# Kernel tuning notes

Hardware: AMD Instinct MI355X
Metric: run time of the kernel (lower is better)

The kernel has to match this reference:

```python
import jax, jax.numpy as jnp
import numpy as np

N_NODES = 100000
N_EDGES = 1600000
D = 128
N_LAYERS = 4
N_GRAPHS = 512


def setup_inputs() -> dict:
    key = jax.random.key(0)
    ks = jax.random.split(key, 12)
    x = jax.random.normal(ks[0], (N_NODES, D), dtype=jnp.float32)
    edge_index = jax.random.randint(ks[1], (2, N_EDGES), 0, N_NODES, dtype=jnp.int64)
    batch = jnp.sort(jax.random.randint(ks[2], (N_NODES,), 0, N_GRAPHS, dtype=jnp.int64))
    scale = 1.0 / np.sqrt(D)
    Ws = jax.random.normal(ks[3], (N_LAYERS, D, D), dtype=jnp.float32) * scale
    bs = jnp.zeros((N_LAYERS, D), dtype=jnp.float32)
    mlp_w1 = jax.random.normal(ks[4], (D, 100), dtype=jnp.float32) * scale
    mlp_b1 = jnp.zeros((100,), dtype=jnp.float32)
    mlp_w2 = jax.random.normal(ks[5], (100, 4), dtype=jnp.float32) * (1.0 / np.sqrt(100.0))
    mlp_b2 = jnp.zeros((4,), dtype=jnp.float32)
    return {"x": x, "Ws": Ws, "bs": bs, "mlp_w1": mlp_w1, "mlp_b1": mlp_b1,
            "mlp_w2": mlp_w2, "mlp_b2": mlp_b2, "edge_index": edge_index, "batch": batch}


def _gcn_conv(x, W, b, row, col, norm):
    # x: [N, Din]; W: [Din, Dout]. PyG GCNConv: linear, then normalized scatter-add.
    xw = x @ W                                # [N, Dout]
    msg = xw[row] * norm[:, None]             # gather at source nodes [E', Dout]
    out = jax.ops.segment_sum(msg, col, num_segments=N_NODES)
    return out + b


def reference(x, Ws, bs, mlp_w1, mlp_b1, mlp_w2, mlp_b2, edge_index, batch):
    # Add self-loops and compute symmetric normalization (once; shared by all layers).
    loop = jnp.arange(N_NODES, dtype=edge_index.dtype)
    row = jnp.concatenate([edge_index[0], loop])  # source
    col = jnp.concatenate([edge_index[1], loop])  # target
    deg = jax.ops.segment_sum(jnp.ones_like(col, dtype=x.dtype), col, num_segments=N_NODES)
    dinv = jnp.where(deg > 0, jax.lax.rsqrt(deg), 0.0)
    norm = dinv[row] * dinv[col]              # [E']

    h = x
    for i in range(N_LAYERS - 1):
        # dropout is identity in eval mode
        h = _gcn_conv(h, Ws[i], bs[i], row, col, norm)
        h = jax.nn.relu(h)
    h = _gcn_conv(h, Ws[-1], bs[-1], row, col, norm)

    # global mean pool over graphs
    sums = jax.ops.segment_sum(h, batch, num_segments=N_GRAPHS)
    counts = jax.ops.segment_sum(jnp.ones((N_NODES,), dtype=h.dtype), batch, num_segments=N_GRAPHS)
    pooled = sums / jnp.maximum(counts, 1.0)[:, None]  # [G, D]

    # MLP head: D -> 100 -> 4 (relu between, dropout identity in eval)
    hid = jax.nn.relu(pooled @ mlp_w1 + mlp_b1)
    pred = hid @ mlp_w2 + mlp_b2
    return pred
```

## Files before the change

### kernel.cpp

```cpp
#include <hip/hip_runtime.h>

#define N_NODES  100000
#define N_EDGES  1600000
#define DIM      128
#define N_GRAPHS 512

#define BW       512
#define NBUCK    ((N_NODES + BW - 1) / BW)
#define CAP      12288
#define NB_CHUNK 4096

typedef short  bf16x8 __attribute__((ext_vector_type(8)));
typedef float  f32x4  __attribute__((ext_vector_type(4)));

__device__ inline ushort f2bf(float f) {
    union { float f; unsigned u; } v; v.f = f;
    unsigned r = v.u + 0x7FFFu + ((v.u >> 16) & 1u);
    return (ushort)(r >> 16);
}
__device__ inline float bf2f_lo(unsigned u) { union { unsigned u; float f; } v; v.u = u << 16; return v.f; }
__device__ inline float bf2f_hi(unsigned u) { union { unsigned u; float f; } v; v.u = u & 0xFFFF0000u; return v.f; }


__global__ __launch_bounds__(256) void setup_kernel(const float* __restrict__ Ws,
                                                    ushort* __restrict__ WT,
                                                    int* __restrict__ bfill,
                                                    int* __restrict__ csr) {
    int idx = blockIdx.x * 256 + threadIdx.x;
    int L = idx >> 14, n = (idx >> 7) & 127, k = idx & 127;
    WT[idx] = f2bf(Ws[(L << 14) + (k << 7) + n]);
    if (blockIdx.x == 0) {
        int t = threadIdx.x;
        if (t < NBUCK) bfill[t] = t * CAP;
        if (t == 255) csr[N_NODES] = N_EDGES;
    }
}


__global__ __launch_bounds__(1024) void bin_kernel(const int* __restrict__ row,
                                                   const int* __restrict__ col,
                                                   int* __restrict__ bfill,
                                                   unsigned* __restrict__ tmp) {
    __shared__ unsigned s_val[NB_CHUNK];
    __shared__ int s_dst[NB_CHUNK];
    __shared__ int s_hist[256], s_scan[256];
    __shared__ int s_excl[NBUCK], s_base[NBUCK], s_cur[NBUCK];
    int t = threadIdx.x;
    int e0 = blockIdx.x * NB_CHUNK;

    if (t < 256) s_hist[t] = 0;
    __syncthreads();
#pragma unroll
    for (int k = 0; k < 4; ++k) {
        int e = e0 + t + k * 1024;
        if (e < N_EDGES) atomicAdd(&s_hist[col[e] >> 9], 1);
    }
    __syncthreads();
    int h = 0;
    if (t < 256) { h = s_hist[t]; s_scan[t] = h; }
    __syncthreads();
    for (int o = 1; o < 256; o <<= 1) {
        int u = 0;
        if (t < 256 && t >= o) u = s_scan[t - o];
        __syncthreads();
        if (t < 256) s_scan[t] += u;
        __syncthreads();
    }
    if (t < NBUCK) {
        int ex = s_scan[t] - h;
        s_excl[t] = ex;
        s_cur[t]  = ex;
        s_base[t] = atomicAdd(&bfill[t], h);
    }
    __syncthreads();
#pragma unroll
    for (int k = 0; k < 4; ++k) {
        int e = e0 + t + k * 1024;
        if (e < N_EDGES) {
            int r = row[e], c = col[e];
            int b = c >> 9;
            int p = atomicAdd(&s_cur[b], 1);
            int dst = s_base[b] + (p - s_excl[b]);
            int lim = (b + 1) * CAP;
            if (dst >= lim) dst = lim - 1;
            s_val[p] = ((unsigned)(c & (BW - 1)) << 17) | (unsigned)r;
            s_dst[p] = dst;
        }
    }
    __syncthreads();
    int sc = N_EDGES - e0; if (sc > NB_CHUNK) sc = NB_CHUNK;
#pragma unroll
    for (int k = 0; k < 4; ++k) {
        int j = t + k * 1024;
        if (j < sc) tmp[s_dst[j]] = s_val[j];
    }
}

__global__ __launch_bounds__(1024) void sort_kernel(const unsigned* __restrict__ tmp,
                                                    const int* __restrict__ bfill,
                                                    int* __restrict__ csr,
                                                    float* __restrict__ dinv,
                                                    int* __restrict__ ssrc) {
    __shared__ int s_cnt[BW];
    __shared__ int s_pair[256];
    __shared__ int s_off[BW];
    __shared__ int s_cur[BW];
    __shared__ int s_bb[256];
    __shared__ int s_stage[CAP];
    int b = blockIdx.x, t = threadIdx.x;
    int wbeg = b * BW;
    int wn = N_NODES - wbeg; if (wn > BW) wn = BW;
    int nE = bfill[b] - b * CAP; if (nE > CAP) nE = CAP;
    const unsigned* T = tmp + (size_t)b * CAP;

    if (t < 256) {
        int c0 = 0;
        if (t < NBUCK) {
            c0 = bfill[t] - t * CAP;
            if (c0 > CAP) c0 = CAP;
        }
        s_bb[t] = c0;
    }
    __syncthreads();
    for (int o = 1; o < 256; o <<= 1) {
        int u = 0;
        if (t < 256 && t >= o) u = s_bb[t - o];
        __syncthreads();
        if (t < 256) s_bb[t] += u;
        __syncthreads();
    }
    int base = s_bb[b] - nE;

    for (int i = t; i < BW; i += 1024) s_cnt[i] = 0;
    __syncthreads();
    for (int i = t; i < nE; i += 1024) atomicAdd(&s_cnt[T[i] >> 17], 1);
    __syncthreads();
    int a0 = 0, a1 = 0;
    if (t < 256) { a0 = s_cnt[2 * t]; a1 = s_cnt[2 * t + 1]; s_pair[t] = a0 + a1; }
    __syncthreads();
    for (int o = 1; o < 256; o <<= 1) {
        int u = 0;
        if (t < 256 && t >= o) u = s_pair[t - o];
        __syncthreads();
        if (t < 256) s_pair[t] += u;
        __syncthreads();
    }
    if (t < 256) {
        int pre = s_pair[t] - (a0 + a1);
        s_off[2 * t] = pre;      s_off[2 * t + 1] = pre + a0;
        s_cur[2 * t] = pre;      s_cur[2 * t + 1] = pre + a0;
    }
    __syncthreads();
    for (int i = t; i < wn; i += 1024) {
        csr[wbeg + i]  = base + s_off[i];
        dinv[wbeg + i] = rsqrtf((float)(s_cnt[i] + 1));
    }
    for (int i = t; i < nE; i += 1024) {
        unsigned v = T[i];
        int p = atomicAdd(&s_cur[v >> 17], 1);
        s_stage[p] = (int)(v & 0x1FFFFu);
    }
    __syncthreads();
    for (int i = t; i < nE; i += 1024) ssrc[base + i] = s_stage[i];
}


__global__ __launch_bounds__(256) void cvt_x(const float* __restrict__ x,
                                             const float* __restrict__ dinv,
                                             ushort* __restrict__ xb,
                                             const int* __restrict__ batch,
                                             int* __restrict__ gstart) {
    int i = (blockIdx.x * 256 + threadIdx.x) * 4;
    float d = dinv[i >> 7];
    float4 v = *(const float4*)(x + i);
    ushort4 o;
    o.x = f2bf(v.x * d); o.y = f2bf(v.y * d); o.z = f2bf(v.z * d); o.w = f2bf(v.w * d);
    *(ushort4*)(xb + i) = o;

    int n = blockIdx.x * 256 + threadIdx.x;
    if (n < N_NODES) {
        int b  = batch[n];
        int bp = (n == 0) ? -1 : batch[n - 1];
        for (int g = bp + 1; g <= b; ++g) gstart[g] = n;
        if (n == N_NODES - 1) {
            for (int g = b + 1; g <= N_GRAPHS; ++g) gstart[g] = N_NODES;
        }
    }
}

#define ACC8(vv) do { \
    acc[0] += bf2f_lo((vv).x); acc[1] += bf2f_hi((vv).x); \
    acc[2] += bf2f_lo((vv).y); acc[3] += bf2f_hi((vv).y); \
    acc[4] += bf2f_lo((vv).z); acc[5] += bf2f_hi((vv).z); \
    acc[6] += bf2f_lo((vv).w); acc[7] += bf2f_hi((vv).w); } while (0)

__global__ __launch_bounds__(512) void layer_kernel(const ushort* __restrict__ g,
                                                    const ushort* __restrict__ WT,
                                                    const float* __restrict__ bias,
                                                    const float* __restrict__ dinv,
                                                    const int* __restrict__ csr,
                                                    const int* __restrict__ ssrc,
                                                    ushort* __restrict__ out,
                                                    int mode) {
    __shared__ ushort sW[128 * 128];
    __shared__ ushort sA[8][16 * 128];
    int t = threadIdx.x;
    int m0blk = blockIdx.x * 128;

    {
#pragma unroll
        for (int j = 0; j < 4; ++j) {
            int idx = t + j * 512;
            int r = idx >> 4, c = idx & 15;
            uint4 v = *(const uint4*)(WT + (size_t)r * 128 + c * 8);
            *(uint4*)(sW + r * 128 + ((c + r) & 15) * 8) = v;
        }
    }
    __syncthreads();

    int wv   = t >> 6;
    int lane = t & 63;
    int q    = lane >> 4;
    int l    = lane & 15;
    int mw   = m0blk + wv * 16;
    ushort* sAw = sA[wv];
    const uint4* hp = (const uint4*)g;

#pragma unroll 1
    for (int i = 0; i < 4; ++i) {
        int row  = q * 4 + i;
        int node = mw + row;
        float acc[8];
#pragma unroll
        for (int z = 0; z < 8; ++z) acc[z] = 0.f;
        if (node < N_NODES) {
            uint4 v = hp[(size_t)node * 16 + l];
            acc[0] = bf2f_lo(v.x); acc[1] = bf2f_hi(v.x);
            acc[2] = bf2f_lo(v.y); acc[3] = bf2f_hi(v.y);
            acc[4] = bf2f_lo(v.z); acc[5] = bf2f_hi(v.z);
            acc[6] = bf2f_lo(v.w); acc[7] = bf2f_hi(v.w);
            int e = csr[node], end = csr[node + 1];
            for (; e + 7 < end; e += 8) {
                int s0 = ssrc[e],     s1 = ssrc[e + 1], s2 = ssrc[e + 2], s3 = ssrc[e + 3];
                int s4 = ssrc[e + 4], s5 = ssrc[e + 5], s6 = ssrc[e + 6], s7 = ssrc[e + 7];
                uint4 v0 = hp[(size_t)s0 * 16 + l];
                uint4 v1 = hp[(size_t)s1 * 16 + l];
                uint4 v2 = hp[(size_t)s2 * 16 + l];
                uint4 v3 = hp[(size_t)s3 * 16 + l];
                uint4 v4 = hp[(size_t)s4 * 16 + l];
                uint4 v5 = hp[(size_t)s5 * 16 + l];
                uint4 v6 = hp[(size_t)s6 * 16 + l];
                uint4 v7 = hp[(size_t)s7 * 16 + l];
                ACC8(v0); ACC8(v1); ACC8(v2); ACC8(v3);
                ACC8(v4); ACC8(v5); ACC8(v6); ACC8(v7);
            }
            for (; e + 1 < end; e += 2) {
                int s0 = ssrc[e], s1 = ssrc[e + 1];
                uint4 v0 = hp[(size_t)s0 * 16 + l];
                uint4 v1 = hp[(size_t)s1 * 16 + l];
                ACC8(v0); ACC8(v1);
            }
            if (e < end) {
                int s = ssrc[e];
                uint4 v1 = hp[(size_t)s * 16 + l];
                ACC8(v1);
            }
            float d = dinv[node];
#pragma unroll
            for (int z = 0; z < 8; ++z) acc[z] *= d;
        }
        uint4 ov;
        ov.x = (uint)f2bf(acc[0]) | ((uint)f2bf(acc[1]) << 16);
        ov.y = (uint)f2bf(acc[2]) | ((uint)f2bf(acc[3]) << 16);
        ov.z = (uint)f2bf(acc[4]) | ((uint)f2bf(acc[5]) << 16);
        ov.w = (uint)f2bf(acc[6]) | ((uint)f2bf(acc[7]) << 16);
        *(uint4*)(sAw + row * 128 + ((l + row) & 15) * 8) = ov;
    }

    f32x4 facc[8];
#pragma unroll
    for (int n = 0; n < 8; ++n) facc[n] = (f32x4){0.f, 0.f, 0.f, 0.f};
#pragma unroll
    for (int ki = 0; ki < 4; ++ki) {
        int ca = ki * 4 + q;
        bf16x8 a = *(const bf16x8*)(sAw + l * 128 + ((ca + l) & 15) * 8);
#pragma unroll
        for (int n = 0; n < 8; ++n) {
            int rB = n * 16 + l;
            bf16x8 b = *(const bf16x8*)(sW + rB * 128 + ((ca + rB) & 15) * 8);
            facc[n] = __builtin_amdgcn_mfma_f32_16x16x32_bf16(a, b, facc[n], 0, 0, 0);
        }
    }

    {
        int lr0 = q * 4;
        float sc[4];
#pragma unroll
        for (int r = 0; r < 4; ++r) {
            int m = mw + lr0 + r;
            sc[r] = (mode && m < N_NODES) ? dinv[m] : 1.0f;
        }
#pragma unroll
        for (int n = 0; n < 8; ++n) {
            int col = n * 16 + l;
            float bv = bias[col];
            int c = col >> 3;
#pragma unroll
            for (int r = 0; r < 4; ++r) {
                int lr = lr0 + r;
                float v = facc[n][r] + bv;
                if (mode) v = fmaxf(v, 0.f) * sc[r];
                sAw[lr * 128 + ((c + lr) & 15) * 8 + (col & 7)] = f2bf(v);
            }
        }
    }
#pragma unroll
    for (int j = 0; j < 4; ++j) {
        int idx = lane + j * 64;
        int lr = idx >> 4, c = idx & 15;
        int m = mw + lr;
        if (m < N_NODES) {
            uint4 v = *(const uint4*)(sAw + lr * 128 + ((c + lr) & 15) * 8);
            *(uint4*)(out + (size_t)m * 128 + c * 8) = v;
        }
    }
}


__global__ __launch_bounds__(256) void pool_mlp(const ushort* __restrict__ h,
                                                const int* __restrict__ gstart,
                                                const float* __restrict__ w1,
                                                const float* __restrict__ b1,
                                                const float* __restrict__ w2,
                                                const float* __restrict__ b2,
                                                float* __restrict__ out) {
    __shared__ float part[4][128];
    __shared__ float mean[128];
    __shared__ float hid[100];
    int g = blockIdx.x;
    int s = gstart[g], e2 = gstart[g + 1];
    int p     = threadIdx.x & 63;
    int which = threadIdx.x >> 6;
    const uint* hu = (const uint*)h;

    float a0 = 0.f, a1 = 0.f;
    for (int n = s + which; n < e2; n += 4) {
        uint v = hu[(size_t)n * 64 + p];
        a0 += bf2f_lo(v);
        a1 += bf2f_hi(v);
    }
    part[which][2 * p]     = a0;
    part[which][2 * p + 1] = a1;
    __syncthreads();
    if (which == 0) {
        float c = fmaxf((float)(e2 - s), 1.0f);
        mean[2 * p]     = (part[0][2 * p] + part[1][2 * p] + part[2][2 * p] + part[3][2 * p]) / c;
        mean[2 * p + 1] = (part[0][2 * p + 1] + part[1][2 * p + 1] + part[2][2 * p + 1] + part[3][2 * p + 1]) / c;
    }
    __syncthreads();
    int t = threadIdx.x;
    if (t < 100) {
        float s1 = b1[t];
        for (int k = 0; k < 128; ++k) s1 = fmaf(mean[k], w1[k * 100 + t], s1);
        hid[t] = fmaxf(s1, 0.f);
    }
    __syncthreads();
    if (t < 4) {
        float s2 = b2[t];
        for (int j = 0; j < 100; ++j) s2 = fmaf(hid[j], w2[j * 4 + t], s2);
        out[(size_t)g * 4 + t] = s2;
    }
}


extern "C" void kernel_launch(void* const* d_in, const int* in_sizes, int n_in,
                              void* d_out, int out_size, void* d_ws, size_t ws_size,
                              hipStream_t stream) {
    const float* x   = (const float*)d_in[0];
    const float* Ws  = (const float*)d_in[1];
    const float* bs  = (const float*)d_in[2];
    const float* w1  = (const float*)d_in[3];
    const float* b1  = (const float*)d_in[4];
    const float* w2  = (const float*)d_in[5];
    const float* b2  = (const float*)d_in[6];
    const int*   ei  = (const int*)d_in[7];
    const int*   bat = (const int*)d_in[8];
    float* outp = (float*)d_out;

    char* p = (char*)d_ws;
    auto take = [&](size_t bytes) -> void* {
        void* r = (void*)p;
        p += (bytes + 255) & ~(size_t)255;
        return r;
    };
    int*      csr    = (int*)take((size_t)(N_NODES + 1) * 4);
    float*    dinv   = (float*)take((size_t)N_NODES * 4);
    int*      bfill  = (int*)take((size_t)NBUCK * 4);
    unsigned* tmp    = (unsigned*)take((size_t)NBUCK * CAP * 4);
    int*      ssrc   = (int*)take((size_t)N_EDGES * 4);
    ushort*   xb     = (ushort*)take((size_t)N_NODES * 128 * 2);
    ushort*   hbA    = (ushort*)take((size_t)N_NODES * 128 * 2);
    ushort*   hbB    = (ushort*)take((size_t)N_NODES * 128 * 2);
    ushort*   WT     = (ushort*)take((size_t)4 * 128 * 128 * 2);
    int*      gstart = (int*)take((size_t)(N_GRAPHS + 1) * 4);

    const int* row = ei;
    const int* col = ei + N_EDGES;

    setup_kernel<<<256, 256, 0, stream>>>(Ws, WT, bfill, csr);
    bin_kernel<<<(N_EDGES + NB_CHUNK - 1) / NB_CHUNK, 1024, 0, stream>>>(row, col, bfill, tmp);
    sort_kernel<<<NBUCK, 1024, 0, stream>>>(tmp, bfill, csr, dinv, ssrc);
    cvt_x<<<12500, 256, 0, stream>>>(x, dinv, xb, bat, gstart);

    const ushort* hin = xb;
    ushort* hout = hbA;
    for (int L = 0; L < 4; ++L) {
        layer_kernel<<<(N_NODES + 127) / 128, 512, 0, stream>>>(
            hin, WT + (size_t)L * 128 * 128, bs + (size_t)L * 128, dinv,
            csr, ssrc, hout, (L < 3) ? 1 : 0);
        hin = hout;
        hout = (hout == hbA) ? hbB : hbA;
    }
    pool_mlp<<<N_GRAPHS, 256, 0, stream>>>(hin, gstart, w1, b1, w2, b2, outp);
}
```

Baseline: 450.7 us.

## Merge front-end kernels, fuse mean pooling into last layer, scale by dinv in gather

Binning, x conversion to bf16 and weight transposition now run as one front kernel with block-range dispatch, so the cvt_x launch no longer waits on the sort. Because x is now converted before dinv exists, layer 0 applies the source dinv per edge inside the gather. The last layer no longer writes its output; it segment-sums rows per graph into a float accumulator with atomics, and a small MLP head kernel reads those sums. This trades the final activation write and the pool kernel's re-read for global atomics and an extra dinv load per edge in layer 0.

```diff
diff --git a/kernel.cpp b/kernel.cpp
--- a/kernel.cpp
+++ b/kernel.cpp
@@ -10,6 +10,10 @@
 #define CAP      12288
 #define NB_CHUNK 4096
 
+#define FB_BIN   ((N_EDGES + NB_CHUNK - 1) / NB_CHUNK)
+#define FB_CVT   3125
+#define FB_WT    64
+
 typedef short  bf16x8 __attribute__((ext_vector_type(8)));
 typedef float  f32x4  __attribute__((ext_vector_type(4)));
 
@@ -20,79 +24,93 @@
 }
 __device__ inline float bf2f_lo(unsigned u) { union { unsigned u; float f; } v; v.u = u << 16; return v.f; }
 __device__ inline float bf2f_hi(unsigned u) { union { unsigned u; float f; } v; v.u = u & 0xFFFF0000u; return v.f; }
-
-
-__global__ __launch_bounds__(256) void setup_kernel(const float* __restrict__ Ws,
-                                                    ushort* __restrict__ WT,
-                                                    int* __restrict__ bfill,
-                                                    int* __restrict__ csr) {
-    int idx = blockIdx.x * 256 + threadIdx.x;
-    int L = idx >> 14, n = (idx >> 7) & 127, k = idx & 127;
-    WT[idx] = f2bf(Ws[(L << 14) + (k << 7) + n]);
-    if (blockIdx.x == 0) {
-        int t = threadIdx.x;
-        if (t < NBUCK) bfill[t] = t * CAP;
-        if (t == 255) csr[N_NODES] = N_EDGES;
-    }
-}
-
-
-__global__ __launch_bounds__(1024) void bin_kernel(const int* __restrict__ row,
-                                                   const int* __restrict__ col,
-                                                   int* __restrict__ bfill,
-                                                   unsigned* __restrict__ tmp) {
+__device__ inline float bf2f_s(ushort u)    { union { unsigned u; float f; } v; v.u = (unsigned)u << 16; return v.f; }
+
+__global__ __launch_bounds__(1024) void front_kernel(const int* __restrict__ row,
+                                                     const int* __restrict__ col,
+                                                     int* __restrict__ bfill,
+                                                     unsigned* __restrict__ tmp,
+                                                     const float* __restrict__ x,
+                                                     ushort* __restrict__ xb,
+                                                     const int* __restrict__ batch,
+                                                     int* __restrict__ gstart,
+                                                     const float* __restrict__ Ws,
+                                                     ushort* __restrict__ WT) {
     __shared__ unsigned s_val[NB_CHUNK];
     __shared__ int s_dst[NB_CHUNK];
     __shared__ int s_hist[256], s_scan[256];
     __shared__ int s_excl[NBUCK], s_base[NBUCK], s_cur[NBUCK];
     int t = threadIdx.x;
-    int e0 = blockIdx.x * NB_CHUNK;
-
-    if (t < 256) s_hist[t] = 0;
-    __syncthreads();
-#pragma unroll
-    for (int k = 0; k < 4; ++k) {
-        int e = e0 + t + k * 1024;
-        if (e < N_EDGES) atomicAdd(&s_hist[col[e] >> 9], 1);
-    }
-    __syncthreads();
-    int h = 0;
-    if (t < 256) { h = s_hist[t]; s_scan[t] = h; }
-    __syncthreads();
-    for (int o = 1; o < 256; o <<= 1) {
-        int u = 0;
-        if (t < 256 && t >= o) u = s_scan[t - o];
-        __syncthreads();
-        if (t < 256) s_scan[t] += u;
-        __syncthreads();
-    }
-    if (t < NBUCK) {
-        int ex = s_scan[t] - h;
-        s_excl[t] = ex;
-        s_cur[t]  = ex;
-        s_base[t] = atomicAdd(&bfill[t], h);
-    }
-    __syncthreads();
-#pragma unroll
-    for (int k = 0; k < 4; ++k) {
-        int e = e0 + t + k * 1024;
-        if (e < N_EDGES) {
-            int r = row[e], c = col[e];
-            int b = c >> 9;
-            int p = atomicAdd(&s_cur[b], 1);
-            int dst = s_base[b] + (p - s_excl[b]);
-            int lim = (b + 1) * CAP;
-            if (dst >= lim) dst = lim - 1;
-            s_val[p] = ((unsigned)(c & (BW - 1)) << 17) | (unsigned)r;
-            s_dst[p] = dst;
-        }
-    }
-    __syncthreads();
-    int sc = N_EDGES - e0; if (sc > NB_CHUNK) sc = NB_CHUNK;
-#pragma unroll
-    for (int k = 0; k < 4; ++k) {
-        int j = t + k * 1024;
-        if (j < sc) tmp[s_dst[j]] = s_val[j];
+    int bk = blockIdx.x;
+
+    if (bk < FB_BIN) {
+        int e0 = bk * NB_CHUNK;
+        if (t < 256) s_hist[t] = 0;
+        __syncthreads();
+#pragma unroll
+        for (int k = 0; k < 4; ++k) {
+            int e = e0 + t + k * 1024;
+            if (e < N_EDGES) atomicAdd(&s_hist[col[e] >> 9], 1);
+        }
+        __syncthreads();
+        int h = 0;
+        if (t < 256) { h = s_hist[t]; s_scan[t] = h; }
+        __syncthreads();
+        for (int o = 1; o < 256; o <<= 1) {
+            int u = 0;
+            if (t < 256 && t >= o) u = s_scan[t - o];
+            __syncthreads();
+            if (t < 256) s_scan[t] += u;
+            __syncthreads();
+        }
+        if (t < NBUCK) {
+            int ex = s_scan[t] - h;
+            s_excl[t] = ex;
+            s_cur[t]  = ex;
+            s_base[t] = atomicAdd(&bfill[t], h);
+        }
+        __syncthreads();
+#pragma unroll
+        for (int k = 0; k < 4; ++k) {
+            int e = e0 + t + k * 1024;
+            if (e < N_EDGES) {
+                int r = row[e], c = col[e];
+                int b = c >> 9;
+                int p = atomicAdd(&s_cur[b], 1);
+                int dst = b * CAP + s_base[b] + (p - s_excl[b]);
+                int lim = (b + 1) * CAP;
+                if (dst >= lim) dst = lim - 1;
+                s_val[p] = ((unsigned)(c & (BW - 1)) << 17) | (unsigned)r;
+                s_dst[p] = dst;
+            }
+        }
+        __syncthreads();
+        int sc = N_EDGES - e0; if (sc > NB_CHUNK) sc = NB_CHUNK;
+#pragma unroll
+        for (int k = 0; k < 4; ++k) {
+            int j = t + k * 1024;
+            if (j < sc) tmp[s_dst[j]] = s_val[j];
+        }
+    } else if (bk < FB_BIN + FB_CVT) {
+        int idx = (bk - FB_BIN) * 1024 + t;
+        int i = idx * 4;
+        float4 v = *(const float4*)(x + i);
+        ushort4 o;
+        o.x = f2bf(v.x); o.y = f2bf(v.y); o.z = f2bf(v.z); o.w = f2bf(v.w);
+        *(ushort4*)(xb + i) = o;
+        int n = idx;
+        if (n < N_NODES) {
+            int b  = batch[n];
+            int bp = (n == 0) ? -1 : batch[n - 1];
+            for (int g = bp + 1; g <= b; ++g) gstart[g] = n;
+            if (n == N_NODES - 1) {
+                for (int g = b + 1; g <= N_GRAPHS; ++g) gstart[g] = N_NODES;
+            }
+        }
+    } else {
+        int idx = (bk - FB_BIN - FB_CVT) * 1024 + t;
+        int L = idx >> 14, n = (idx >> 7) & 127, k = idx & 127;
+        WT[idx] = f2bf(Ws[(L << 14) + (k << 7) + n]);
     }
 }
 
@@ -110,13 +128,15 @@
     int b = blockIdx.x, t = threadIdx.x;
     int wbeg = b * BW;
     int wn = N_NODES - wbeg; if (wn > BW) wn = BW;
-    int nE = bfill[b] - b * CAP; if (nE > CAP) nE = CAP;
+    int nE = bfill[b]; if (nE > CAP) nE = CAP;
     const unsigned* T = tmp + (size_t)b * CAP;
+
+    if (b == 0 && t == 0) csr[N_NODES] = N_EDGES;
 
     if (t < 256) {
         int c0 = 0;
         if (t < NBUCK) {
-            c0 = bfill[t] - t * CAP;
+            c0 = bfill[t];
             if (c0 > CAP) c0 = CAP;
         }
         s_bb[t] = c0;
@@ -162,30 +182,6 @@
     }
     __syncthreads();
     for (int i = t; i < nE; i += 1024) ssrc[base + i] = s_stage[i];
-}
-
-
-__global__ __launch_bounds__(256) void cvt_x(const float* __restrict__ x,
-                                             const float* __restrict__ dinv,
-                                             ushort* __restrict__ xb,
-                                             const int* __restrict__ batch,
-                                             int* __restrict__ gstart) {
-    int i = (blockIdx.x * 256 + threadIdx.x) * 4;
-    float d = dinv[i >> 7];
-    float4 v = *(const float4*)(x + i);
-    ushort4 o;
-    o.x = f2bf(v.x * d); o.y = f2bf(v.y * d); o.z = f2bf(v.z * d); o.w = f2bf(v.w * d);
-    *(ushort4*)(xb + i) = o;
-
-    int n = blockIdx.x * 256 + threadIdx.x;
-    if (n < N_NODES) {
-        int b  = batch[n];
-        int bp = (n == 0) ? -1 : batch[n - 1];
-        for (int g = bp + 1; g <= b; ++g) gstart[g] = n;
-        if (n == N_NODES - 1) {
-            for (int g = b + 1; g <= N_GRAPHS; ++g) gstart[g] = N_NODES;
-        }
-    }
 }
 
 #define ACC8(vv) do { \
@@ -193,6 +189,54 @@
     acc[2] += bf2f_lo((vv).y); acc[3] += bf2f_hi((vv).y); \
     acc[4] += bf2f_lo((vv).z); acc[5] += bf2f_hi((vv).z); \
     acc[6] += bf2f_lo((vv).w); acc[7] += bf2f_hi((vv).w); } while (0)
+
+#define ACC8S(vv, dd) do { \
+    acc[0] = fmaf(bf2f_lo((vv).x), dd, acc[0]); acc[1] = fmaf(bf2f_hi((vv).x), dd, acc[1]); \
+    acc[2] = fmaf(bf2f_lo((vv).y), dd, acc[2]); acc[3] = fmaf(bf2f_hi((vv).y), dd, acc[3]); \
+    acc[4] = fmaf(bf2f_lo((vv).z), dd, acc[4]); acc[5] = fmaf(bf2f_hi((vv).z), dd, acc[5]); \
+    acc[6] = fmaf(bf2f_lo((vv).w), dd, acc[6]); acc[7] = fmaf(bf2f_hi((vv).w), dd, acc[7]); } while (0)
+
+template<bool GS>
+__device__ __forceinline__ void gather_edges(const uint4* __restrict__ hp,
+                                             const int* __restrict__ ssrc,
+                                             const float* __restrict__ dv,
+                                             int e, int end, int l, float* acc) {
+    for (; e + 7 < end; e += 8) {
+        int s0 = ssrc[e],     s1 = ssrc[e + 1], s2 = ssrc[e + 2], s3 = ssrc[e + 3];
+        int s4 = ssrc[e + 4], s5 = ssrc[e + 5], s6 = ssrc[e + 6], s7 = ssrc[e + 7];
+        float d0 = 0.f, d1 = 0.f, d2 = 0.f, d3 = 0.f, d4 = 0.f, d5 = 0.f, d6 = 0.f, d7 = 0.f;
+        if (GS) { d0 = dv[s0]; d1 = dv[s1]; d2 = dv[s2]; d3 = dv[s3];
+                  d4 = dv[s4]; d5 = dv[s5]; d6 = dv[s6]; d7 = dv[s7]; }
+        uint4 v0 = hp[(size_t)s0 * 16 + l];
+        uint4 v1 = hp[(size_t)s1 * 16 + l];
+        uint4 v2 = hp[(size_t)s2 * 16 + l];
+        uint4 v3 = hp[(size_t)s3 * 16 + l];
+        uint4 v4 = hp[(size_t)s4 * 16 + l];
+        uint4 v5 = hp[(size_t)s5 * 16 + l];
+        uint4 v6 = hp[(size_t)s6 * 16 + l];
+        uint4 v7 = hp[(size_t)s7 * 16 + l];
+        if (GS) { ACC8S(v0, d0); ACC8S(v1, d1); ACC8S(v2, d2); ACC8S(v3, d3);
+                  ACC8S(v4, d4); ACC8S(v5, d5); ACC8S(v6, d6); ACC8S(v7, d7); }
+        else    { ACC8(v0); ACC8(v1); ACC8(v2); ACC8(v3);
+                  ACC8(v4); ACC8(v5); ACC8(v6); ACC8(v7); }
+    }
+    for (; e + 1 < end; e += 2) {
+        int s0 = ssrc[e], s1 = ssrc[e + 1];
+        float d0 = 0.f, d1 = 0.f;
+        if (GS) { d0 = dv[s0]; d1 = dv[s1]; }
+        uint4 v0 = hp[(size_t)s0 * 16 + l];
+        uint4 v1 = hp[(size_t)s1 * 16 + l];
+        if (GS) { ACC8S(v0, d0); ACC8S(v1, d1); }
+        else    { ACC8(v0); ACC8(v1); }
+    }
+    if (e < end) {
+        int s = ssrc[e];
+        float d0 = 0.f;
+        if (GS) d0 = dv[s];
+        uint4 v1 = hp[(size_t)s * 16 + l];
+        if (GS) ACC8S(v1, d0); else ACC8(v1);
+    }
+}
 
 __global__ __launch_bounds__(512) void layer_kernel(const ushort* __restrict__ g,
                                                     const ushort* __restrict__ WT,
@@ -201,6 +245,8 @@
                                                     const int* __restrict__ csr,
                                                     const int* __restrict__ ssrc,
                                                     ushort* __restrict__ out,
+                                                    const int* __restrict__ batch,
+                                                    float* __restrict__ accum,
                                                     int mode) {
     __shared__ ushort sW[128 * 128];
     __shared__ ushort sA[8][16 * 128];
@@ -235,36 +281,11 @@
         for (int z = 0; z < 8; ++z) acc[z] = 0.f;
         if (node < N_NODES) {
             uint4 v = hp[(size_t)node * 16 + l];
-            acc[0] = bf2f_lo(v.x); acc[1] = bf2f_hi(v.x);
-            acc[2] = bf2f_lo(v.y); acc[3] = bf2f_hi(v.y);
-            acc[4] = bf2f_lo(v.z); acc[5] = bf2f_hi(v.z);
-            acc[6] = bf2f_lo(v.w); acc[7] = bf2f_hi(v.w);
+            if (mode & 2) { float ds = dinv[node]; ACC8S(v, ds); }
+            else          { ACC8(v); }
             int e = csr[node], end = csr[node + 1];
-            for (; e + 7 < end; e += 8) {
-                int s0 = ssrc[e],     s1 = ssrc[e + 1], s2 = ssrc[e + 2], s3 = ssrc[e + 3];
-                int s4 = ssrc[e + 4], s5 = ssrc[e + 5], s6 = ssrc[e + 6], s7 = ssrc[e + 7];
-                uint4 v0 = hp[(size_t)s0 * 16 + l];
-                uint4 v1 = hp[(size_t)s1 * 16 + l];
-                uint4 v2 = hp[(size_t)s2 * 16 + l];
-                uint4 v3 = hp[(size_t)s3 * 16 + l];
-                uint4 v4 = hp[(size_t)s4 * 16 + l];
-                uint4 v5 = hp[(size_t)s5 * 16 + l];
-                uint4 v6 = hp[(size_t)s6 * 16 + l];
-                uint4 v7 = hp[(size_t)s7 * 16 + l];
-                ACC8(v0); ACC8(v1); ACC8(v2); ACC8(v3);
-                ACC8(v4); ACC8(v5); ACC8(v6); ACC8(v7);
-            }
-            for (; e + 1 < end; e += 2) {
-                int s0 = ssrc[e], s1 = ssrc[e + 1];
-                uint4 v0 = hp[(size_t)s0 * 16 + l];
-                uint4 v1 = hp[(size_t)s1 * 16 + l];
-                ACC8(v0); ACC8(v1);
-            }
-            if (e < end) {
-                int s = ssrc[e];
-                uint4 v1 = hp[(size_t)s * 16 + l];
-                ACC8(v1);
-            }
+            if (mode & 2) gather_edges<true>(hp, ssrc, dinv, e, end, l, acc);
+            else          gather_edges<false>(hp, ssrc, dinv, e, end, l, acc);
             float d = dinv[node];
 #pragma unroll
             for (int z = 0; z < 8; ++z) acc[z] *= d;
@@ -294,11 +315,12 @@
 
     {
         int lr0 = q * 4;
+        bool rp = (mode & 1);
         float sc[4];
 #pragma unroll
         for (int r = 0; r < 4; ++r) {
             int m = mw + lr0 + r;
-            sc[r] = (mode && m < N_NODES) ? dinv[m] : 1.0f;
+            sc[r] = (rp && m < N_NODES) ? dinv[m] : 1.0f;
         }
 #pragma unroll
         for (int n = 0; n < 8; ++n) {
@@ -309,56 +331,58 @@
             for (int r = 0; r < 4; ++r) {
                 int lr = lr0 + r;
                 float v = facc[n][r] + bv;
-                if (mode) v = fmaxf(v, 0.f) * sc[r];
+                if (rp) v = fmaxf(v, 0.f) * sc[r];
                 sAw[lr * 128 + ((c + lr) & 15) * 8 + (col & 7)] = f2bf(v);
             }
         }
     }
-#pragma unroll
-    for (int j = 0; j < 4; ++j) {
-        int idx = lane + j * 64;
-        int lr = idx >> 4, c = idx & 15;
-        int m = mw + lr;
-        if (m < N_NODES) {
-            uint4 v = *(const uint4*)(sAw + lr * 128 + ((c + lr) & 15) * 8);
-            *(uint4*)(out + (size_t)m * 128 + c * 8) = v;
-        }
-    }
-}
-
-
-__global__ __launch_bounds__(256) void pool_mlp(const ushort* __restrict__ h,
+
+    if (!(mode & 4)) {
+#pragma unroll
+        for (int j = 0; j < 4; ++j) {
+            int idx = lane + j * 64;
+            int lr = idx >> 4, c = idx & 15;
+            int m = mw + lr;
+            if (m < N_NODES) {
+                uint4 v = *(const uint4*)(sAw + lr * 128 + ((c + lr) & 15) * 8);
+                *(uint4*)(out + (size_t)m * 128 + c * 8) = v;
+            }
+        }
+    } else {
+        __syncthreads();
+        int col = t & 127, rg = t >> 7;
+        int nrows = N_NODES - m0blk; if (nrows > 128) nrows = 128;
+        float sum = 0.f; int cg = -1;
+        for (int r = rg; r < nrows; r += 4) {
+            int m = m0blk + r;
+            int gg = batch[m];
+            const ushort* sp = sA[r >> 4];
+            float v = bf2f_s(sp[(r & 15) * 128 + (((col >> 3) + (r & 15)) & 15) * 8 + (col & 7)]);
+            if (gg != cg) {
+                if (cg >= 0) atomicAdd(&accum[cg * 128 + col], sum);
+                cg = gg; sum = v;
+            } else {
+                sum += v;
+            }
+        }
+        if (cg >= 0) atomicAdd(&accum[cg * 128 + col], sum);
+    }
+}
+
+
+__global__ __launch_bounds__(128) void mlp_head(const float* __restrict__ accum,
                                                 const int* __restrict__ gstart,
                                                 const float* __restrict__ w1,
                                                 const float* __restrict__ b1,
                                                 const float* __restrict__ w2,
                                                 const float* __restrict__ b2,
                                                 float* __restrict__ out) {
-    __shared__ float part[4][128];
     __shared__ float mean[128];
     __shared__ float hid[100];
-    int g = blockIdx.x;
-    int s = gstart[g], e2 = gstart[g + 1];
-    int p     = threadIdx.x & 63;
-    int which = threadIdx.x >> 6;
-    const uint* hu = (const uint*)h;
-
-    float a0 = 0.f, a1 = 0.f;
-    for (int n = s + which; n < e2; n += 4) {
-        uint v = hu[(size_t)n * 64 + p];
-        a0 += bf2f_lo(v);
-        a1 += bf2f_hi(v);
-    }
-    part[which][2 * p]     = a0;
-    part[which][2 * p + 1] = a1;
-    __syncthreads();
-    if (which == 0) {
-        float c = fmaxf((float)(e2 - s), 1.0f);
-        mean[2 * p]     = (part[0][2 * p] + part[1][2 * p] + part[2][2 * p] + part[3][2 * p]) / c;
-        mean[2 * p + 1] = (part[0][2 * p + 1] + part[1][2 * p + 1] + part[2][2 * p + 1] + part[3][2 * p + 1]) / c;
-    }
-    __syncthreads();
-    int t = threadIdx.x;
+    int g = blockIdx.x, t = threadIdx.x;
+    float c = fmaxf((float)(gstart[g + 1] - gstart[g]), 1.0f);
+    mean[t] = accum[g * 128 + t] / c;
+    __syncthreads();
     if (t < 100) {
         float s1 = b1[t];
         for (int k = 0; k < 128; ++k) s1 = fmaf(mean[k], w1[k * 100 + t], s1);
@@ -403,23 +427,27 @@
     ushort*   hbB    = (ushort*)take((size_t)N_NODES * 128 * 2);
     ushort*   WT     = (ushort*)take((size_t)4 * 128 * 128 * 2);
     int*      gstart = (int*)take((size_t)(N_GRAPHS + 1) * 4);
+    float*    accum  = (float*)take((size_t)N_GRAPHS * DIM * 4);
 
     const int* row = ei;
     const int* col = ei + N_EDGES;
 
-    setup_kernel<<<256, 256, 0, stream>>>(Ws, WT, bfill, csr);
-    bin_kernel<<<(N_EDGES + NB_CHUNK - 1) / NB_CHUNK, 1024, 0, stream>>>(row, col, bfill, tmp);
+    hipMemsetAsync(bfill, 0, (size_t)NBUCK * 4, stream);
+    hipMemsetAsync(accum, 0, (size_t)N_GRAPHS * DIM * 4, stream);
+
+    front_kernel<<<FB_BIN + FB_CVT + FB_WT, 1024, 0, stream>>>(
+        row, col, bfill, tmp, x, xb, bat, gstart, Ws, WT);
     sort_kernel<<<NBUCK, 1024, 0, stream>>>(tmp, bfill, csr, dinv, ssrc);
-    cvt_x<<<12500, 256, 0, stream>>>(x, dinv, xb, bat, gstart);
 
     const ushort* hin = xb;
     ushort* hout = hbA;
     for (int L = 0; L < 4; ++L) {
+        int mode = (L == 0) ? 3 : (L < 3) ? 1 : 4;
         layer_kernel<<<(N_NODES + 127) / 128, 512, 0, stream>>>(
             hin, WT + (size_t)L * 128 * 128, bs + (size_t)L * 128, dinv,
-            csr, ssrc, hout, (L < 3) ? 1 : 0);
+            csr, ssrc, hout, bat, accum, mode);
         hin = hout;
         hout = (hout == hbA) ? hbB : hbA;
     }
-    pool_mlp<<<N_GRAPHS, 256, 0, stream>>>(hin, gstart, w1, b1, w2, b2, outp);
-}
+    mlp_head<<<N_GRAPHS, 128, 0, stream>>>(accum, gstart, w1, b1, w2, b2, outp);
+}
```

Result: slower. 460.0 us (+2.1%).
